# Optimization experiments

Hardware: AMD Instinct MI355X
Metric: run time of the kernel (lower is better)

## Reference

```python
import jax, jax.numpy as jnp
import numpy as np

B, N, L, D, H, GOUT = 256, 307, 12, 16, 8, 32


def pos_encoding():
    # positional_encoding(X, 16): P[1, L, D]
    pos = jnp.arange(L, dtype=jnp.float32)[:, None]
    div = jnp.power(10000.0, jnp.arange(0, D, 2, dtype=jnp.float32) / D)
    ang = pos / div  # [L, D/2]
    P = jnp.zeros((L, D), dtype=jnp.float32)
    P = P.at[:, 0::2].set(jnp.sin(ang)).at[:, 1::2].set(jnp.cos(ang))
    return P[None]  # [1, L, D]


def setup_inputs() -> dict:
    key = jax.random.key(0)
    ks = jax.random.split(key, 24)
    s = 0.02
    inp = {
        "flow_x": jax.random.normal(ks[0], (B, N, L), dtype=jnp.float32),
        "day_cyc": jax.random.randint(ks[1], (B, L), 0, 289),
        "week_cyc": jax.random.randint(ks[2], (B, L), 0, 8),
        "adj": (jax.random.uniform(ks[3], (N, N)) < 0.03).astype(jnp.float32),
        "day_emb": jax.random.normal(ks[4], (289, D), dtype=jnp.float32) * s,
        "week_emb": jax.random.normal(ks[5], (8, D), dtype=jnp.float32) * s,
        "Wq": jax.random.normal(ks[6], (D, D), dtype=jnp.float32) * s,
        "bq": jnp.zeros((D,), jnp.float32),
        "Wk": jax.random.normal(ks[7], (D, D), dtype=jnp.float32) * s,
        "bk": jnp.zeros((D,), jnp.float32),
        "Wv": jax.random.normal(ks[8], (D, D), dtype=jnp.float32) * s,
        "bv": jnp.zeros((D,), jnp.float32),
        "Wo": jax.random.normal(ks[9], (D, D), dtype=jnp.float32) * s,
        "bo": jnp.zeros((D,), jnp.float32),
        "Wg": jax.random.normal(ks[10], (1, GOUT), dtype=jnp.float32) * s,
        "Wt": jax.random.normal(ks[11], (D, GOUT), dtype=jnp.float32) * s,
        "bg": jnp.zeros((GOUT,), jnp.float32),
        "W1": jax.random.normal(ks[12], (N, GOUT, 8), dtype=jnp.float32) * s,
        "b1": jnp.zeros((N, 8), jnp.float32),
        "W2": jax.random.normal(ks[13], (N, 8, 1), dtype=jnp.float32) * s,
        "b2": jnp.zeros((N, 1), jnp.float32),
    }
    return inp


def dyn_graph(flow_x):
    # his_win[:, 0:12] = flow_x[0]; his_win[:, 11+b] = flow_x[b, :, -1] for b>=1
    his = jnp.concatenate([flow_x[0], flow_x[1:, :, -1].T], axis=1)  # [N, 11+B]
    sq = jnp.sum(his * his, axis=1)
    d2 = sq[:, None] + sq[None, :] - 2.0 * (his @ his.T)
    return jnp.sqrt(jnp.maximum(d2, 0.0))  # [N, N] euclidean distances


def reference(flow_x, day_cyc, week_cyc, adj, day_emb, week_emb,
              Wq, bq, Wk, bk, Wv, bv, Wo, bo, Wg, Wt, bg, W1, b1, W2, b2):
    hd = D // H  # head dim = 2
    fun_graph = dyn_graph(flow_x)                          # [N, N]
    pe = pos_encoding()                                    # [1, L, D]
    te = day_emb[day_cyc] + week_emb[week_cyc]             # [B, L, D]
    x_t = flow_x[..., None] + pe[:, None] + te[:, None]    # [B, N, L, D]

    # multi-head self-attention over time axis (8 heads, dim 16)
    def heads(x, W, b):
        return (x @ W + b).reshape(x.shape[0], x.shape[1], L, H, hd)
    q, k, v = heads(x_t, Wq, bq), heads(x_t, Wk, bk), heads(x_t, Wv, bv)
    logits = jnp.einsum('bnlhd,bnmhd->bnhlm', q, k) / jnp.sqrt(jnp.float32(hd))
    att = jnp.einsum('bnhlm,bnmhd->bnlhd', jax.nn.softmax(logits, axis=-1), v)
    att = att.reshape(flow_x.shape[0], N, L, D) @ Wo + bo
    x_tcn = x_t + att                                      # [B, N, L, D]

    # graph-temporal block: dynamic-graph message passing + static-graph mix
    A_dyn = jax.nn.softmax(-fun_graph, axis=-1)            # closer vertices weigh more
    A_st = adj / (jnp.sum(adj, axis=-1, keepdims=True) + 1.0)
    x_gcn = flow_x[..., None]                              # [B, N, L, 1]
    hid = jax.nn.relu(
        jnp.einsum('nm,bmlc->bnlc', A_dyn, x_gcn @ Wg)
        + jnp.einsum('nm,bmlc->bnlc', A_st, x_tcn @ Wt)
        + bg)                                              # [B, N, L, 32]

    # per-vertex 2-layer MLPs, batched over N (replaces the Python loop)
    h1 = jax.nn.relu(jnp.einsum('bnlc,nco->bnlo', hid, W1) + b1[None, :, None])
    out = jnp.einsum('bnlo,noz->bnlz', h1, W2) + b2[None, :, None]
    return out[..., 0]                                     # [B, N, 12]
```

## Files before the change

kernel.cpp:

```cpp
#include <hip/hip_runtime.h>
#include <hip/hip_bf16.h>
#include <math.h>

#define NB 256
#define NN 307
#define NBN 78592
#define LL 12
#define DDIM 16
#define HISW 268
#define HIS4 67
#define NBRCAP 64
#define AGRP 15
#define ADTS 308

#define OFF_XTCN 0u
#define OFF_G1   15089664u
#define OFF_ADT  16032768u
#define OFF_TEQ  16127456u
#define OFF_HIS  16176608u
#define OFF_TEK  16176608u
#define OFF_NW   16258896u
#define OFF_NIDX 16278544u
#define OFF_NCNT 16298192u
#define OFF_TEV  16298512u
#define OFF_TEO  16347664u

__device__ inline float4 mkf4(float a, float b, float c, float d) {
    float4 r; r.x = a; r.y = b; r.z = c; r.w = d; return r;
}

__global__ void his_kernel(const float* __restrict__ flow, float* __restrict__ his) {
    int e = blockIdx.x * 256 + threadIdx.x;
    if (e >= NN * HISW) return;
    int n = e / HISW, j = e - n * HISW;
    float v = 0.f;
    if (j < LL) v = flow[n * LL + j];
    else if (j < 267) v = flow[((j - 11) * NN + n) * LL + 11];
    his[e] = v;
}

__global__ __launch_bounds__(256) void te_kernel(
    const int* __restrict__ dayc, const int* __restrict__ weekc,
    const float* __restrict__ demb, const float* __restrict__ wemb,
    const float* __restrict__ Wq, const float* __restrict__ bq,
    const float* __restrict__ Wk, const float* __restrict__ bk,
    const float* __restrict__ Wv, const float* __restrict__ bv,
    const float* __restrict__ bo,
    float* __restrict__ TEQ, float* __restrict__ TEK,
    float* __restrict__ TEV, float* __restrict__ TEO) {
    __shared__ float sTE[16][16];
    int t = threadIdx.x, r = t >> 4, d = t & 15;
    int row = blockIdx.x * 16 + r;
    int b = row / LL, l = row - b * LL;
    int dc = dayc[b * LL + l], wc = weekc[b * LL + l];
    int i = d >> 1;
    float ang = (float)l * powf(10000.f, -0.125f * (float)i);
    float pe = (d & 1) ? cosf(ang) : sinf(ang);
    float te = demb[dc * DDIM + d] + wemb[wc * DDIM + d] + pe;
    sTE[r][d] = te;
    __syncthreads();
    float aq = bq[d], ak = bk[d], av = bv[d];
#pragma unroll
    for (int e = 0; e < 16; e++) {
        float x = sTE[r][e];
        aq += x * Wq[e * 16 + d];
        ak += x * Wk[e * 16 + d];
        av += x * Wv[e * 16 + d];
    }
    TEQ[row * 16 + d] = aq * 0.70710678118654752f;
    TEK[row * 16 + d] = ak;
    TEV[row * 16 + d] = av;
    TEO[row * 16 + d] = te + bo[d];
}

__global__ __launch_bounds__(256) void adyn_kernel(const float* __restrict__ his,
                                                   float* __restrict__ AdT) {
    __shared__ float4 sh[HIS4];
    __shared__ float red[256];
    int n = blockIdx.x, t = threadIdx.x;
    if (t < HIS4) sh[t] = reinterpret_cast<const float4*>(his)[n * HIS4 + t];
    __syncthreads();

    float e0 = 0.f, e1 = 0.f, lsum = 0.f;
    {
        const float4* row = reinterpret_cast<const float4*>(his) + t * HIS4;
        float4 acc = mkf4(0.f, 0.f, 0.f, 0.f);
        for (int j = 0; j < HIS4; j++) {
            float4 a = sh[j], b = row[j];
            float dx = a.x - b.x, dy = a.y - b.y, dz = a.z - b.z, dw = a.w - b.w;
            acc.x += dx * dx; acc.y += dy * dy; acc.z += dz * dz; acc.w += dw * dw;
        }
        float d2 = (acc.x + acc.y) + (acc.z + acc.w);
        e0 = __expf(-sqrtf(fmaxf(d2, 0.f)));
        lsum += e0;
    }
    int m1 = t + 256;
    if (m1 < NN) {
        const float4* row = reinterpret_cast<const float4*>(his) + m1 * HIS4;
        float4 acc = mkf4(0.f, 0.f, 0.f, 0.f);
        for (int j = 0; j < HIS4; j++) {
            float4 a = sh[j], b = row[j];
            float dx = a.x - b.x, dy = a.y - b.y, dz = a.z - b.z, dw = a.w - b.w;
            acc.x += dx * dx; acc.y += dy * dy; acc.z += dz * dz; acc.w += dw * dw;
        }
        float d2 = (acc.x + acc.y) + (acc.z + acc.w);
        e1 = __expf(-sqrtf(fmaxf(d2, 0.f)));
        lsum += e1;
    }
    red[t] = lsum;
    __syncthreads();
    for (int s = 128; s > 0; s >>= 1) {
        if (t < s) red[t] += red[t + s];
        __syncthreads();
    }
    float inv = 1.f / red[0];
    AdT[t * ADTS + n] = e0 * inv;
    if (m1 < NN) AdT[m1 * ADTS + n] = e1 * inv;
}

__global__ __launch_bounds__(64) void nbr_kernel(const float* __restrict__ adj,
                                                 int* __restrict__ ncnt,
                                                 int* __restrict__ nidx,
                                                 float* __restrict__ nw) {
    int n = blockIdx.x, t = threadIdx.x;
    float rs = 0.f;
    for (int m0 = 0; m0 < NN; m0 += 64) {
        int m = m0 + t;
        if (m < NN) rs += adj[n * NN + m];
    }
    for (int off = 32; off > 0; off >>= 1) rs += __shfl_xor(rs, off);
    float inv = 1.f / (rs + 1.f);
    int c = 0;
    for (int m0 = 0; m0 < NN; m0 += 64) {
        int m = m0 + t;
        float a = (m < NN) ? adj[n * NN + m] : 0.f;
        bool p = (a != 0.f);
        unsigned long long mask = __ballot(p);
        int pos = __popcll(mask & ((1ull << t) - 1ull));
        if (p && (c + pos) < NBRCAP) {
            nidx[n * NBRCAP + c + pos] = m;
            nw[n * NBRCAP + c + pos] = a * inv;
        }
        c += (int)__popcll(mask);
    }
    if (t == 0) ncnt[n] = c < NBRCAP ? c : NBRCAP;
}

__global__ __launch_bounds__(192, 5) void attn_kernel(
    const float* __restrict__ flow,
    const float* __restrict__ TEQ, const float* __restrict__ TEK,
    const float* __restrict__ TEV, const float* __restrict__ TEO,
    const float* __restrict__ Wq, const float* __restrict__ Wk,
    const float* __restrict__ Wv, const float* __restrict__ Wo,
    float* __restrict__ xtcn) {
    __shared__ __align__(16) float sWo[256];
    __shared__ __align__(16) float sWs[48];
    __shared__ __align__(16) float sKV[2][AGRP][LL][20];

    const int t = threadIdx.x;
    for (int id = t; id < 256; id += 192) sWo[id] = Wo[id];
    if (t < 48) {
        int mat = t >> 4, d = t & 15;
        const float* W = (mat == 0) ? Wq : (mat == 1) ? Wk : Wv;
        float s = 0.f;
#pragma unroll
        for (int e = 0; e < 16; e++) s += W[e * 16 + d];
        sWs[t] = (mat == 0) ? s * 0.70710678118654752f : s;
    }

    const int g = t / LL, l = t - g * LL;
    const int bn = blockIdx.x * AGRP + g;
    const bool act = (t < AGRP * LL) && (bn < NBN);

    float f = 0.f;
    float tq[16], tk[16], tv[16];
    int row = 0;
    if (act) {
        const int b = bn / NN;
        row = b * LL + l;
        f = flow[bn * LL + l];
        const float4* q4 = reinterpret_cast<const float4*>(TEQ + row * 16);
        const float4* k4 = reinterpret_cast<const float4*>(TEK + row * 16);
        const float4* v4 = reinterpret_cast<const float4*>(TEV + row * 16);
#pragma unroll
        for (int j = 0; j < 4; j++) {
            float4 a = q4[j]; tq[4 * j] = a.x; tq[4 * j + 1] = a.y; tq[4 * j + 2] = a.z; tq[4 * j + 3] = a.w;
            float4 bb = k4[j]; tk[4 * j] = bb.x; tk[4 * j + 1] = bb.y; tk[4 * j + 2] = bb.z; tk[4 * j + 3] = bb.w;
            float4 c = v4[j]; tv[4 * j] = c.x; tv[4 * j + 1] = c.y; tv[4 * j + 2] = c.z; tv[4 * j + 3] = c.w;
        }
    }
    __syncthreads();

    float q[16];
    if (act) {
        float k[16], v[16];
        const float4* ws4 = reinterpret_cast<const float4*>(sWs);
#pragma unroll
        for (int j = 0; j < 4; j++) {
            float4 wq = ws4[j], wk = ws4[4 + j], wv = ws4[8 + j];
            q[4 * j] = tq[4 * j] + f * wq.x;       q[4 * j + 1] = tq[4 * j + 1] + f * wq.y;
            q[4 * j + 2] = tq[4 * j + 2] + f * wq.z; q[4 * j + 3] = tq[4 * j + 3] + f * wq.w;
            k[4 * j] = tk[4 * j] + f * wk.x;       k[4 * j + 1] = tk[4 * j + 1] + f * wk.y;
            k[4 * j + 2] = tk[4 * j + 2] + f * wk.z; k[4 * j + 3] = tk[4 * j + 3] + f * wk.w;
            v[4 * j] = tv[4 * j] + f * wv.x;       v[4 * j + 1] = tv[4 * j + 1] + f * wv.y;
            v[4 * j + 2] = tv[4 * j + 2] + f * wv.z; v[4 * j + 3] = tv[4 * j + 3] + f * wv.w;
        }
        float4* kd = reinterpret_cast<float4*>(&sKV[0][g][l][0]);
        float4* vd = reinterpret_cast<float4*>(&sKV[1][g][l][0]);
#pragma unroll
        for (int j = 0; j < 4; j++) {
            kd[j] = mkf4(k[4 * j], k[4 * j + 1], k[4 * j + 2], k[4 * j + 3]);
            vd[j] = mkf4(v[4 * j], v[4 * j + 1], v[4 * j + 2], v[4 * j + 3]);
        }
    }
    __syncthreads();

    if (act) {
        float att[16];
#pragma unroll
        for (int h = 0; h < 8; h++) {
            float qx = q[2 * h], qy = q[2 * h + 1];
            float s[LL];
            float sum = 0.f;
#pragma unroll
            for (int m = 0; m < LL; m++) {
                float2 kk = *reinterpret_cast<const float2*>(&sKV[0][g][m][2 * h]);
                s[m] = __expf(qx * kk.x + qy * kk.y);
                sum += s[m];
            }
            float a0 = 0.f, a1 = 0.f;
#pragma unroll
            for (int m = 0; m < LL; m++) {
                float2 vv = *reinterpret_cast<const float2*>(&sKV[1][g][m][2 * h]);
                a0 += s[m] * vv.x; a1 += s[m] * vv.y;
            }
            float inv = 1.f / sum;
            att[2 * h] = a0 * inv; att[2 * h + 1] = a1 * inv;
        }
        float o[16];
        const float4* to4 = reinterpret_cast<const float4*>(TEO + row * 16);
#pragma unroll
        for (int j = 0; j < 4; j++) {
            float4 a = to4[j];
            o[4 * j] = a.x; o[4 * j + 1] = a.y; o[4 * j + 2] = a.z; o[4 * j + 3] = a.w;
        }
#pragma unroll
        for (int e = 0; e < 16; e++) {
            float ae = att[e];
            const float4* wo = reinterpret_cast<const float4*>(&sWo[e * 16]);
#pragma unroll
            for (int j = 0; j < 4; j++) {
                float4 w = wo[j];
                o[4 * j] += ae * w.x; o[4 * j + 1] += ae * w.y;
                o[4 * j + 2] += ae * w.z; o[4 * j + 3] += ae * w.w;
            }
        }
        float4* dst = reinterpret_cast<float4*>(xtcn) + (size_t)bn * 48 + l * 4;
#pragma unroll
        for (int j = 0; j < 4; j++) {
            dst[j] = mkf4(o[4 * j] + f, o[4 * j + 1] + f, o[4 * j + 2] + f, o[4 * j + 3] + f);
        }
    }
}

__global__ __launch_bounds__(256) void g1_kernel(const float* __restrict__ flow,
                                                 const float* __restrict__ AdT,
                                                 float* __restrict__ G1) {
    __shared__ float sflow[NN * LL];
    int b = blockIdx.x, nt = blockIdx.y, t = threadIdx.x;
    const float* fb = flow + (size_t)b * (NN * LL);
    for (int e = t; e < NN * LL; e += 256) sflow[e] = fb[e];
    __syncthreads();

    int lane = t & 63, lq = t >> 6;
    int n = nt * 128 + 2 * lane;
    int l0 = lq * 3;
    float a00 = 0.f, a01 = 0.f, a02 = 0.f, a10 = 0.f, a11 = 0.f, a12 = 0.f;
#pragma unroll 4
    for (int m = 0; m < NN; m++) {
        float2 w = reinterpret_cast<const float2*>(AdT + (size_t)m * ADTS + nt * 128)[lane];
        float f0 = sflow[m * LL + l0];
        float f1 = sflow[m * LL + l0 + 1];
        float f2 = sflow[m * LL + l0 + 2];
        a00 += w.x * f0; a01 += w.x * f1; a02 += w.x * f2;
        a10 += w.y * f0; a11 += w.y * f1; a12 += w.y * f2;
    }
    if (n < NN) {
        float* dst = G1 + ((size_t)b * NN + n) * LL + l0;
        dst[0] = a00; dst[1] = a01; dst[2] = a02;
    }
    if (n + 1 < NN) {
        float* dst = G1 + ((size_t)b * NN + n + 1) * LL + l0;
        dst[0] = a10; dst[1] = a11; dst[2] = a12;
    }
}

__global__ __launch_bounds__(256) void final_kernel(
    const float* __restrict__ xtcn, const float* __restrict__ G1,
    const float* __restrict__ Wg, const float* __restrict__ Wt,
    const float* __restrict__ bg, const float* __restrict__ W1,
    const float* __restrict__ b1, const float* __restrict__ W2,
    const float* __restrict__ b2, const int* __restrict__ ncnt,
    const int* __restrict__ nidx, const float* __restrict__ nw,
    float* __restrict__ out) {
    __shared__ __align__(16) float sWt[512];
    __shared__ __align__(16) float sW1[256];
    __shared__ __align__(16) float sWg[32];
    __shared__ __align__(16) float sBg[32];
    __shared__ float sB1[8], sW2[8];
    __shared__ __align__(16) float sY[4][192];
    __shared__ __align__(16) float4 sHID[4][96];
    __shared__ float sH1[4][96];

    int t = threadIdx.x;
    int n = blockIdx.x;
    int w = t >> 6, t64 = t & 63;
    int b = blockIdx.y * 4 + w;

    sW1[t] = W1[n * 256 + t];
    sWt[t] = Wt[t];
    sWt[t + 256] = Wt[t + 256];
    if (t < 32) sWg[t] = Wg[t];
    else if (t < 64) sBg[t - 32] = bg[t - 32];
    else if (t < 72) sB1[t - 64] = b1[n * 8 + (t - 64)];
    else if (t < 80) sW2[t - 72] = W2[n * 8 + (t - 72)];
    float b2v = b2[n];
    int cnt = ncnt[n];
    __syncthreads();

    float y0 = 0.f, y1 = 0.f, y2 = 0.f;
    const float* base = xtcn + (size_t)b * NN * 192;
    int i = 0;
    for (; i + 1 < cnt; i += 2) {
        int ma = nidx[n * NBRCAP + i], mb = nidx[n * NBRCAP + i + 1];
        float wa = nw[n * NBRCAP + i], wb = nw[n * NBRCAP + i + 1];
        const float* sa = base + ma * 192;
        const float* sb = base + mb * 192;
        float p0 = sa[t64], p1 = sa[t64 + 64], p2 = sa[t64 + 128];
        float q0 = sb[t64], q1 = sb[t64 + 64], q2 = sb[t64 + 128];
        y0 += wa * p0 + wb * q0; y1 += wa * p1 + wb * q1; y2 += wa * p2 + wb * q2;
    }
    if (i < cnt) {
        int ma = nidx[n * NBRCAP + i];
        float wa = nw[n * NBRCAP + i];
        const float* sa = base + ma * 192;
        y0 += wa * sa[t64]; y1 += wa * sa[t64 + 64]; y2 += wa * sa[t64 + 128];
    }
    sY[w][t64] = y0; sY[w][t64 + 64] = y1; sY[w][t64 + 128] = y2;
    __syncthreads();

#pragma unroll
    for (int p = 0; p < 2; p++) {
        int c = t64 + p * 64;
        if (c < 96) {
            int l = c >> 3, j = c & 7;
            float g = G1[((size_t)b * NN + n) * LL + l];
            float4 wg = reinterpret_cast<const float4*>(sWg)[j];
            float4 acc = reinterpret_cast<const float4*>(sBg)[j];
            acc.x += g * wg.x; acc.y += g * wg.y; acc.z += g * wg.z; acc.w += g * wg.w;
            const float4* yr = reinterpret_cast<const float4*>(&sY[w][l * 16]);
            float4 v0 = yr[0], v1 = yr[1], v2 = yr[2], v3 = yr[3];
            float ye[16] = {v0.x, v0.y, v0.z, v0.w, v1.x, v1.y, v1.z, v1.w,
                            v2.x, v2.y, v2.z, v2.w, v3.x, v3.y, v3.z, v3.w};
#pragma unroll
            for (int d = 0; d < 16; d++) {
                float4 wt = reinterpret_cast<const float4*>(sWt)[d * 8 + j];
                acc.x += ye[d] * wt.x; acc.y += ye[d] * wt.y;
                acc.z += ye[d] * wt.z; acc.w += ye[d] * wt.w;
            }
            acc.x = fmaxf(acc.x, 0.f); acc.y = fmaxf(acc.y, 0.f);
            acc.z = fmaxf(acc.z, 0.f); acc.w = fmaxf(acc.w, 0.f);
            sHID[w][c] = acc;
        }
    }
    __syncthreads();

#pragma unroll
    for (int p = 0; p < 2; p++) {
        int o = t64 + p * 64;
        if (o < 96) {
            int l = o >> 3, oo = o & 7;
            float acc = sB1[oo];
            float he[32];
#pragma unroll
            for (int k = 0; k < 8; k++) {
                float4 hv = sHID[w][l * 8 + k];
                he[4 * k + 0] = hv.x; he[4 * k + 1] = hv.y;
                he[4 * k + 2] = hv.z; he[4 * k + 3] = hv.w;
            }
#pragma unroll
            for (int c = 0; c < 32; c++) acc += he[c] * sW1[c * 8 + oo];
            sH1[w][o] = fmaxf(acc, 0.f);
        }
    }
    __syncthreads();

    if (t64 < LL) {
        float acc = b2v;
#pragma unroll
        for (int o = 0; o < 8; o++) acc += sH1[w][t64 * 8 + o] * sW2[o];
        out[((size_t)b * NN + n) * LL + t64] = acc;
    }
}

extern "C" void kernel_launch(void* const* d_in, const int* in_sizes, int n_in,
                              void* d_out, int out_size, void* d_ws, size_t ws_size,
                              hipStream_t stream) {
    const float* flow = (const float*)d_in[0];
    const int* dayc   = (const int*)d_in[1];
    const int* weekc  = (const int*)d_in[2];
    const float* adj  = (const float*)d_in[3];
    const float* demb = (const float*)d_in[4];
    const float* wemb = (const float*)d_in[5];
    const float* Wq = (const float*)d_in[6];  const float* bq = (const float*)d_in[7];
    const float* Wk = (const float*)d_in[8];  const float* bk = (const float*)d_in[9];
    const float* Wv = (const float*)d_in[10]; const float* bv = (const float*)d_in[11];
    const float* Wo = (const float*)d_in[12]; const float* bo = (const float*)d_in[13];
    const float* Wg = (const float*)d_in[14]; const float* Wt = (const float*)d_in[15];
    const float* bg = (const float*)d_in[16];
    const float* W1 = (const float*)d_in[17]; const float* b1 = (const float*)d_in[18];
    const float* W2 = (const float*)d_in[19]; const float* b2 = (const float*)d_in[20];
    float* out = (float*)d_out;
    float* ws  = (float*)d_ws;

    float* xtcn = ws + OFF_XTCN;
    float* G1   = ws + OFF_G1;
    float* AdT  = ws + OFF_ADT;
    float* TEQ  = ws + OFF_TEQ;
    float* TEK  = ws + OFF_TEK;
    float* TEV  = ws + OFF_TEV;
    float* TEO  = ws + OFF_TEO;
    float* his  = ws + OFF_HIS;
    float* nw   = ws + OFF_NW;
    int*   nidx = (int*)(ws + OFF_NIDX);
    int*   ncnt = (int*)(ws + OFF_NCNT);

    his_kernel<<<(NN * HISW + 255) / 256, 256, 0, stream>>>(flow, his);
    adyn_kernel<<<NN, 256, 0, stream>>>(his, AdT);
    te_kernel<<<(NB * LL) / 16, 256, 0, stream>>>(dayc, weekc, demb, wemb,
                                                  Wq, bq, Wk, bk, Wv, bv, bo,
                                                  TEQ, TEK, TEV, TEO);
    nbr_kernel<<<NN, 64, 0, stream>>>(adj, ncnt, nidx, nw);
    attn_kernel<<<(NBN + AGRP - 1) / AGRP, 192, 0, stream>>>(flow, TEQ, TEK, TEV, TEO,
                                                             Wq, Wk, Wv, Wo, xtcn);
    g1_kernel<<<dim3(NB, 3), 256, 0, stream>>>(flow, AdT, G1);
    final_kernel<<<dim3(NN, 64), 256, 0, stream>>>(xtcn, G1, Wg, Wt, bg, W1, b1, W2, b2,
                                                   ncnt, nidx, nw, out);
}
```

Baseline: 293.7 us.

## Store x_tcn intermediate as bf16 and pad shared-memory rows in final kernel

The attention kernel now rounds its [B,N,L,16] output to bf16 and packs pairs into 32-bit words, which halves the size of the large intermediate buffer. The final kernel gathers neighbour rows as packed uint2 loads, widens them back to float, and accumulates in fp32 using 48 lanes per warp. Shared-memory rows for sY and sHID are padded (stride 20 and 10) to cut bank conflicts. The aim is to reduce global write and gather traffic, at the cost of bf16 rounding error in x_tcn.

```diff
diff --git a/kernel.cpp b/kernel.cpp
--- a/kernel.cpp
+++ b/kernel.cpp
@@ -152,7 +152,7 @@
     const float* __restrict__ TEV, const float* __restrict__ TEO,
     const float* __restrict__ Wq, const float* __restrict__ Wk,
     const float* __restrict__ Wv, const float* __restrict__ Wo,
-    float* __restrict__ xtcn) {
+    unsigned short* __restrict__ xtcn) {
     __shared__ __align__(16) float sWo[256];
     __shared__ __align__(16) float sWs[48];
     __shared__ __align__(16) float sKV[2][AGRP][LL][20];
@@ -255,11 +255,17 @@
                 o[4 * j + 2] += ae * w.z; o[4 * j + 3] += ae * w.w;
             }
         }
-        float4* dst = reinterpret_cast<float4*>(xtcn) + (size_t)bn * 48 + l * 4;
-#pragma unroll
-        for (int j = 0; j < 4; j++) {
-            dst[j] = mkf4(o[4 * j] + f, o[4 * j + 1] + f, o[4 * j + 2] + f, o[4 * j + 3] + f);
-        }
+        unsigned pk[8];
+#pragma unroll
+        for (int j = 0; j < 8; j++) {
+            unsigned u0 = __float_as_uint(o[2 * j] + f) + 0x8000u;
+            unsigned u1 = __float_as_uint(o[2 * j + 1] + f) + 0x8000u;
+            pk[j] = (u0 >> 16) | (u1 & 0xffff0000u);
+        }
+        uint4* dst = reinterpret_cast<uint4*>(xtcn + (size_t)bn * 192 + l * 16);
+        uint4 d0; d0.x = pk[0]; d0.y = pk[1]; d0.z = pk[2]; d0.w = pk[3];
+        uint4 d1; d1.x = pk[4]; d1.y = pk[5]; d1.z = pk[6]; d1.w = pk[7];
+        dst[0] = d0; dst[1] = d1;
     }
 }
 
@@ -296,7 +302,7 @@
 }
 
 __global__ __launch_bounds__(256) void final_kernel(
-    const float* __restrict__ xtcn, const float* __restrict__ G1,
+    const unsigned short* __restrict__ xtcn, const float* __restrict__ G1,
     const float* __restrict__ Wg, const float* __restrict__ Wt,
     const float* __restrict__ bg, const float* __restrict__ W1,
     const float* __restrict__ b1, const float* __restrict__ W2,
@@ -308,8 +314,8 @@
     __shared__ __align__(16) float sWg[32];
     __shared__ __align__(16) float sBg[32];
     __shared__ float sB1[8], sW2[8];
-    __shared__ __align__(16) float sY[4][192];
-    __shared__ __align__(16) float4 sHID[4][96];
+    __shared__ __align__(16) float sY[4][240];
+    __shared__ __align__(16) float4 sHID[4][120];
     __shared__ float sH1[4][96];
 
     int t = threadIdx.x;
@@ -328,25 +334,32 @@
     int cnt = ncnt[n];
     __syncthreads();
 
-    float y0 = 0.f, y1 = 0.f, y2 = 0.f;
-    const float* base = xtcn + (size_t)b * NN * 192;
-    int i = 0;
-    for (; i + 1 < cnt; i += 2) {
-        int ma = nidx[n * NBRCAP + i], mb = nidx[n * NBRCAP + i + 1];
-        float wa = nw[n * NBRCAP + i], wb = nw[n * NBRCAP + i + 1];
-        const float* sa = base + ma * 192;
-        const float* sb = base + mb * 192;
-        float p0 = sa[t64], p1 = sa[t64 + 64], p2 = sa[t64 + 128];
-        float q0 = sb[t64], q1 = sb[t64 + 64], q2 = sb[t64 + 128];
-        y0 += wa * p0 + wb * q0; y1 += wa * p1 + wb * q1; y2 += wa * p2 + wb * q2;
-    }
-    if (i < cnt) {
-        int ma = nidx[n * NBRCAP + i];
-        float wa = nw[n * NBRCAP + i];
-        const float* sa = base + ma * 192;
-        y0 += wa * sa[t64]; y1 += wa * sa[t64 + 64]; y2 += wa * sa[t64 + 128];
-    }
-    sY[w][t64] = y0; sY[w][t64 + 64] = y1; sY[w][t64 + 128] = y2;
+    if (t64 < 48) {
+        float y0 = 0.f, y1 = 0.f, y2 = 0.f, y3 = 0.f;
+        const unsigned short* base = xtcn + (size_t)b * NN * 192;
+        int i = 0;
+        for (; i + 1 < cnt; i += 2) {
+            int ma = nidx[n * NBRCAP + i], mb = nidx[n * NBRCAP + i + 1];
+            float wa = nw[n * NBRCAP + i], wb = nw[n * NBRCAP + i + 1];
+            uint2 pa = reinterpret_cast<const uint2*>(base + ma * 192)[t64];
+            uint2 pb = reinterpret_cast<const uint2*>(base + mb * 192)[t64];
+            y0 += wa * __uint_as_float(pa.x << 16) + wb * __uint_as_float(pb.x << 16);
+            y1 += wa * __uint_as_float(pa.x & 0xffff0000u) + wb * __uint_as_float(pb.x & 0xffff0000u);
+            y2 += wa * __uint_as_float(pa.y << 16) + wb * __uint_as_float(pb.y << 16);
+            y3 += wa * __uint_as_float(pa.y & 0xffff0000u) + wb * __uint_as_float(pb.y & 0xffff0000u);
+        }
+        if (i < cnt) {
+            int ma = nidx[n * NBRCAP + i];
+            float wa = nw[n * NBRCAP + i];
+            uint2 pa = reinterpret_cast<const uint2*>(base + ma * 192)[t64];
+            y0 += wa * __uint_as_float(pa.x << 16);
+            y1 += wa * __uint_as_float(pa.x & 0xffff0000u);
+            y2 += wa * __uint_as_float(pa.y << 16);
+            y3 += wa * __uint_as_float(pa.y & 0xffff0000u);
+        }
+        int l = t64 >> 2, p = (t64 & 3);
+        reinterpret_cast<float4*>(&sY[w][l * 20])[p] = mkf4(y0, y1, y2, y3);
+    }
     __syncthreads();
 
 #pragma unroll
@@ -358,7 +371,7 @@
             float4 wg = reinterpret_cast<const float4*>(sWg)[j];
             float4 acc = reinterpret_cast<const float4*>(sBg)[j];
             acc.x += g * wg.x; acc.y += g * wg.y; acc.z += g * wg.z; acc.w += g * wg.w;
-            const float4* yr = reinterpret_cast<const float4*>(&sY[w][l * 16]);
+            const float4* yr = reinterpret_cast<const float4*>(&sY[w][l * 20]);
             float4 v0 = yr[0], v1 = yr[1], v2 = yr[2], v3 = yr[3];
             float ye[16] = {v0.x, v0.y, v0.z, v0.w, v1.x, v1.y, v1.z, v1.w,
                             v2.x, v2.y, v2.z, v2.w, v3.x, v3.y, v3.z, v3.w};
@@ -370,7 +383,7 @@
             }
             acc.x = fmaxf(acc.x, 0.f); acc.y = fmaxf(acc.y, 0.f);
             acc.z = fmaxf(acc.z, 0.f); acc.w = fmaxf(acc.w, 0.f);
-            sHID[w][c] = acc;
+            sHID[w][l * 10 + j] = acc;
         }
     }
     __syncthreads();
@@ -384,7 +397,7 @@
             float he[32];
 #pragma unroll
             for (int k = 0; k < 8; k++) {
-                float4 hv = sHID[w][l * 8 + k];
+                float4 hv = sHID[w][l * 10 + k];
                 he[4 * k + 0] = hv.x; he[4 * k + 1] = hv.y;
                 he[4 * k + 2] = hv.z; he[4 * k + 3] = hv.w;
             }
@@ -423,7 +436,7 @@
     float* out = (float*)d_out;
     float* ws  = (float*)d_ws;
 
-    float* xtcn = ws + OFF_XTCN;
+    unsigned short* xtcn = (unsigned short*)(ws + 0);
     float* G1   = ws + OFF_G1;
     float* AdT  = ws + OFF_ADT;
     float* TEQ  = ws + OFF_TEQ;
```

Result: no change. 292.2 us (-0.5%).
